# Kernel tuning notes

Measured on AMD Instinct MI355X. Metric: run time of the kernel, lower is better.

## Reference

```python
import jax, jax.numpy as jnp
import numpy as np
import math

D_MODEL = 1024
NUM_HEADS = 16
ALPHA, BETA, K_SCALE, C_THRESHOLD = 0.7, 0.3, 5.0, 0.3
TAU_SCHEDULE = [0.05, 0.05, 0.05, 0.15, 0.25, 0.35, 0.45, 0.55, 0.65, 0.7, 0.75, 0.8]


def setup_inputs() -> dict:
    key = jax.random.key(0)
    ks = jax.random.split(key, 6)
    B, S = 2, 1024
    scale = D_MODEL ** -0.5
    return {
        "x": jax.random.normal(ks[0], (B, S, D_MODEL), dtype=jnp.float32),
        "entropy_prev": jax.random.uniform(ks[1], (B, NUM_HEADS, S, 1), dtype=jnp.float32),
        "Wq": jax.random.normal(ks[2], (D_MODEL, D_MODEL), dtype=jnp.float32) * scale,
        "Wk": jax.random.normal(ks[3], (D_MODEL, D_MODEL), dtype=jnp.float32) * scale,
        "Wv": jax.random.normal(ks[4], (D_MODEL, D_MODEL), dtype=jnp.float32) * scale,
        "Wo": jax.random.normal(ks[5], (D_MODEL, D_MODEL), dtype=jnp.float32) * scale,
        "layer_idx": 4,
    }


def _proj(x, W, B, S, H, Dh):
    # nn.Linear(bias=False): y = x @ W.T ; then [B,S,H,Dh] -> [B,H,S,Dh]
    return jnp.einsum('bsd,ed->bse', x, W).reshape(B, S, H, Dh).transpose(0, 2, 1, 3)


def reference(x, entropy_prev, Wq, Wk, Wv, Wo, layer_idx):
    B, S, _ = x.shape
    H = NUM_HEADS
    Dh = D_MODEL // H
    tau = TAU_SCHEDULE[int(layer_idx)]

    Q = _proj(x, Wq, B, S, H, Dh)
    K = _proj(x, Wk, B, S, H, Dh)
    V = _proj(x, Wv, B, S, H, Dh)

    # raw scores [B,H,S,S]
    scores_raw = jnp.einsum('bhqd,bhkd->bhqk', Q, K) / math.sqrt(Dh)

    # key salience [B,H,1,S]
    sal = jnp.minimum((K * K).sum(axis=-1) / float(Dh), 2.0)
    sal_b = sal[:, :, None, :]

    # WIPER gate [B,H,S,S] (entropy_prev broadcasts over key dim)
    E_t = jax.nn.sigmoid(K_SCALE * (entropy_prev - C_THRESHOLD))
    gate_logit = jnp.clip(E_t * 5.0 + ALPHA * sal_b * 2.0 - BETA * entropy_prev * 1.0, -20.0, 20.0)
    gate = jax.nn.sigmoid(gate_logit)

    mask = gate >= tau
    scores_gated = jnp.where(mask, scores_raw + jnp.log(gate + 1e-8), -jnp.inf)

    best_k_idx = jnp.argmax(scores_raw, axis=-1)  # [B,H,S]
    any_finite = mask.any(axis=-1, keepdims=True)  # [B,H,S,1]

    # safe softmax: degenerate (all -inf) rows replaced by 0s, result discarded below
    attn_raw = jax.nn.softmax(jnp.where(any_finite, scores_gated, 0.0), axis=-1)
    keep_one = jax.nn.one_hot(best_k_idx, S, dtype=x.dtype)
    attn = jnp.where(any_finite, attn_raw, keep_one)

    O = jnp.einsum('bhqk,bhkd->bhqd', attn, V)

    # entropy state: S = log(l) - E[s']
    max_scores = scores_gated.max(axis=-1, keepdims=True)
    shifted = scores_gated - max_scores
    fm = jnp.isfinite(shifted)
    shifted_safe = jnp.where(fm, shifted, 0.0)
    exp_scores = jnp.where(fm, jnp.exp(shifted_safe), 0.0)
    l = jnp.maximum(exp_scores.sum(axis=-1, keepdims=True), 1e-20)
    weighted = (exp_scores * shifted_safe).sum(axis=-1, keepdims=True)
    S_state = jnp.where(any_finite, jnp.log(l) - weighted / l, 0.0)

    out = jnp.einsum('bsd,ed->bse', O.transpose(0, 2, 1, 3).reshape(B, S, D_MODEL), Wo)
    return out, S_state
```

## Files before the change

### kernel.cpp

```cpp
#include <hip/hip_runtime.h>
#include <cstdint>

#define DEVINL __device__ __forceinline__

typedef __attribute__((ext_vector_type(8))) short bf16x8;
typedef __attribute__((ext_vector_type(4))) float f32x4;
typedef __attribute__((ext_vector_type(8))) unsigned short u16x8;
typedef unsigned short u16;
typedef unsigned int u32;

#define MFMA16(a, b, c) __builtin_amdgcn_mfma_f32_16x16x32_bf16(a, b, c, 0, 0, 0)

#define LOG2E 1.4426950408889634f
#define LN2 0.69314718055994531f

DEVINL u16 f2bf(float x) {
  u32 u = __builtin_bit_cast(u32, x);
  u += 0x7FFFu + ((u >> 16) & 1u);
  return (u16)(u >> 16);
}
DEVINL float exp2fast(float x) {
  float r;
  asm("v_exp_f32 %0, %1" : "=v"(r) : "v"(x));
  return r;
}
DEVINL void gload_lds16(const void* g, void* l) {
  __builtin_amdgcn_global_load_lds(
      (const __attribute__((address_space(1))) unsigned int*)g,
      (__attribute__((address_space(3))) unsigned int*)l, 16, 0, 0);
}

__global__ __launch_bounds__(256) void k_prep(const float* __restrict__ x,
                                              const float* __restrict__ Wq,
                                              const float* __restrict__ Wk,
                                              const float* __restrict__ Wv,
                                              const float* __restrict__ Wo,
                                              const float* __restrict__ ent,
                                              u16* __restrict__ xb,
                                              u16* __restrict__ Wb,
                                              u16* __restrict__ Wob,
                                              float* __restrict__ efq) {
  const int bid = blockIdx.x;
  if (bid < 3072) {
    const float* src;
    u16* dst;
    int base;
    if (bid < 1024)      { src = x;  dst = xb;            base = bid; }
    else if (bid < 1536) { src = Wq; dst = Wb;            base = bid - 1024; }
    else if (bid < 2048) { src = Wk; dst = Wb + (1u<<20); base = bid - 1536; }
    else if (bid < 2560) { src = Wv; dst = Wb + (2u<<20); base = bid - 2048; }
    else                 { src = Wo; dst = Wob;           base = bid - 2560; }
    int i = base * 256 + threadIdx.x;
    const float4* s4 = (const float4*)src;
    float4 a = s4[2 * i], b = s4[2 * i + 1];
    u16x8 o;
    o[0] = f2bf(a.x); o[1] = f2bf(a.y); o[2] = f2bf(a.z); o[3] = f2bf(a.w);
    o[4] = f2bf(b.x); o[5] = f2bf(b.y); o[6] = f2bf(b.z); o[7] = f2bf(b.w);
    *(u16x8*)(dst + 8 * i) = o;
  } else {
    int i = (bid - 3072) * 256 + threadIdx.x;
    float e = ent[i];
    float Et = 1.f / (1.f + __expf(-5.f * (e - 0.3f)));
    efq[i] = __expf(-(5.f * Et - 0.3f * e));
  }
}

template <int BM, int BN, int NDIM, int MODE>
__global__ __launch_bounds__(256) void k_gemm(const u16* __restrict__ A,
                                              const u16* __restrict__ Bw,
                                              int Kdim, u16* __restrict__ Qo,
                                              u16* __restrict__ Ko,
                                              u16* __restrict__ Vt,
                                              float* __restrict__ egk_out,
                                              float* __restrict__ Cout) {
  constexpr int MT = BM / 32, NT = BN / 32;
  constexpr int MB = 2048 / BM, NB = NDIM / BN;
  constexpr int CPX = MB * NB / 8;
  __shared__ __align__(16) u16 SM[2][(BM + BN) * 64];
  const int t = threadIdx.x;
  const int lb = (blockIdx.x & 7) * CPX + (blockIdx.x >> 3);
  const int m0 = (lb % MB) * BM, n0 = (lb / MB) * BN;
  const int lane = t & 63, w = t >> 6;
  const int wr = w >> 1, wc = w & 1, lm = lane & 15, lg = lane >> 4;
  const int rs = t >> 3, cs = t & 7;
  f32x4 acc[MT][NT] = {};

#define GSTAGE(buf, kt)                                                        \
  {                                                                            \
    u16* As_ = SM[buf];                                                        \
    u16* Bs_ = SM[buf] + BM * 64;                                              \
    _Pragma("unroll") for (int i = 0; i < BM / 32; ++i) {                      \
      int rr = rs + 32 * i;                                                    \
      gload_lds16(A + (size_t)(m0 + rr) * Kdim + (kt) + ((cs ^ (rr & 7)) * 8), \
                  (char*)As_ + t * 16 + i * 4096);                             \
    }                                                                          \
    _Pragma("unroll") for (int i = 0; i < BN / 32; ++i) {                      \
      int rr = rs + 32 * i;                                                    \
      gload_lds16(Bw + (size_t)(n0 + rr) * Kdim + (kt) + ((cs ^ (rr & 7)) * 8),\
                  (char*)Bs_ + t * 16 + i * 4096);                             \
    }                                                                          \
  }

  GSTAGE(0, 0);
  __syncthreads();
  const int nk = Kdim >> 6;
  for (int ki = 0; ki < nk; ++ki) {
    const int cur = ki & 1;
    if (ki + 1 < nk) GSTAGE(cur ^ 1, (ki + 1) * 64);
    const u16* As = SM[cur];
    const u16* Bs = SM[cur] + BM * 64;
#pragma unroll
    for (int ks = 0; ks < 2; ++ks) {
      bf16x8 af[MT], bfr[NT];
#pragma unroll
      for (int mt = 0; mt < MT; ++mt) {
        int row = wr * (BM / 2) + mt * 16 + lm;
        af[mt] = *(const bf16x8*)((const char*)As + row * 128 +
                                  (((ks * 4 + lg) ^ (row & 7)) << 4));
      }
#pragma unroll
      for (int nt = 0; nt < NT; ++nt) {
        int row = wc * (BN / 2) + nt * 16 + lm;
        bfr[nt] = *(const bf16x8*)((const char*)Bs + row * 128 +
                                   (((ks * 4 + lg) ^ (row & 7)) << 4));
      }
#pragma unroll
      for (int mt = 0; mt < MT; ++mt)
#pragma unroll
        for (int nt = 0; nt < NT; ++nt)
          acc[mt][nt] = MFMA16(af[mt], bfr[nt], acc[mt][nt]);
    }
    __syncthreads();
  }
#undef GSTAGE

  if (MODE == 1) {
#pragma unroll
    for (int mt = 0; mt < MT; ++mt)
#pragma unroll
      for (int nt = 0; nt < NT; ++nt)
#pragma unroll
        for (int r = 0; r < 4; ++r) {
          int m = m0 + wr * (BM / 2) + mt * 16 + lg * 4 + r;
          int n = n0 + wc * (BN / 2) + nt * 16 + lm;
          Cout[(size_t)m * 1024 + n] = acc[mt][nt][r];
        }
    return;
  }

  const int region = n0 >> 10;
  const int b = m0 >> 10, s0 = m0 & 1023;
  if (region < 2) {
    u16* dst = region == 0 ? Qo : Ko;
    const float scl = region == 0 ? 0.125f * LOG2E : 1.f;
#pragma unroll
    for (int mt = 0; mt < MT; ++mt)
#pragma unroll
      for (int nt = 0; nt < NT; ++nt)
#pragma unroll
        for (int r = 0; r < 4; ++r) {
          int m = m0 + wr * (BM / 2) + mt * 16 + lg * 4 + r;
          int n = n0 + wc * (BN / 2) + nt * 16 + lm;
          int e = n & 1023, h = e >> 6, d = e & 63;
          dst[(size_t)(((b << 4) + h) * 1024 + (m & 1023)) * 64 + d] =
              f2bf(acc[mt][nt][r] * scl);
        }
    if (region == 1) {
      int hh = ((n0 - 1024) >> 6) + wc;
#pragma unroll
      for (int mt = 0; mt < MT; ++mt)
#pragma unroll
        for (int r = 0; r < 4; ++r) {
          float ss = 0.f;
#pragma unroll
          for (int nt = 0; nt < NT; ++nt) ss += acc[mt][nt][r] * acc[mt][nt][r];
          ss += __shfl_xor(ss, 1);
          ss += __shfl_xor(ss, 2);
          ss += __shfl_xor(ss, 4);
          ss += __shfl_xor(ss, 8);
          if (lm == 0) {
            int s = s0 + wr * (BM / 2) + mt * 16 + lg * 4 + r;
            float g = 1.4f * fminf(ss * (1.f / 64.f), 2.f);
            egk_out[(size_t)(((b << 4) + hh)) * 1024 + s] = __expf(-g);
          }
        }
    }
  } else {
    u16* tile = SM[0];
#pragma unroll
    for (int half = 0; half < 2; ++half) {
      if (wc == half) {
#pragma unroll
        for (int mt = 0; mt < MT; ++mt)
#pragma unroll
          for (int nt = 0; nt < NT; ++nt)
#pragma unroll
            for (int r = 0; r < 4; ++r) {
              int d = nt * 16 + lm;
              int mloc = wr * (BM / 2) + mt * 16 + lg * 4 + r;
              tile[d * 64 + (mloc ^ ((d & 7) << 3))] = f2bf(acc[mt][nt][r]);
            }
      }
      __syncthreads();
      int hh = ((n0 - 2048) >> 6) + half;
#pragma unroll
      for (int j = 0; j < 2; ++j) {
        int dd = (t >> 3) + 32 * j, mc = t & 7;
        u16x8 v = *(const u16x8*)&tile[dd * 64 + ((mc * 8) ^ ((dd & 7) << 3))];
        *(u16x8*)(Vt + ((size_t)(((b << 4) + hh) * 64 + dd)) * 1024 + s0 + mc * 8) = v;
      }
      __syncthreads();
    }
  }
}

__global__ __launch_bounds__(256, 2) void k_attn(const u16* __restrict__ Q,
                                                 const u16* __restrict__ Kt,
                                                 const u16* __restrict__ Vt,
                                                 const float* __restrict__ efq,
                                                 const float* __restrict__ egk,
                                                 u16* __restrict__ Ob,
                                                 float* __restrict__ Sst) {
  __shared__ __align__(16) u16 Ks[2][128 * 64];
  __shared__ __align__(16) u16 Vs[2][64 * 128];
  __shared__ __align__(16) u32 Ps[4][16][64];
  const int i = blockIdx.x;
  const int lb = ((i & 7) << 6) | (i >> 3);
  const int bh = lb >> 4, qblk = lb & 15;
  const int t = threadIdx.x, lane = t & 63, w = t >> 6;
  const int lm = lane & 15, lg = lane >> 4;
  const int b = bh >> 4, h = bh & 15;
  const size_t bhS = (size_t)bh << 10;
  const int qb = qblk * 64 + w * 16;

#define STAGE(buf, k0)                                                         \
  {                                                                            \
    int rowK = t >> 3, cK = t & 7;                                             \
    int rowV = t >> 4, cV = t & 15;                                            \
    _Pragma("unroll") for (int i2 = 0; i2 < 4; ++i2) {                         \
      int rr = rowK + 32 * i2;                                                 \
      gload_lds16(Kt + (bhS + (k0) + rr) * 64 + ((cK ^ (rr & 7)) * 8),         \
                  (char*)Ks[buf] + t * 16 + i2 * 4096);                        \
      int dd2 = rowV + 16 * i2;                                                \
      gload_lds16(Vt + ((size_t)bh * 64 + dd2) * 1024 + (k0) +                 \
                      ((cV ^ (dd2 & 15)) * 8),                                 \
                  (char*)Vs[buf] + t * 16 + i2 * 4096);                        \
    }                                                                          \
  }

  bf16x8 qf[2];
#pragma unroll
  for (int ks = 0; ks < 2; ++ks)
    qf[ks] = *(const bf16x8*)(Q + (bhS + qb + lm) * 64 + ks * 32 + lg * 8);
  const float efql = efq[bhS + qb + lm];

  f32x4 Oacc[4] = {};
  float m_r = -1e30f, l_r = 0.f, W_r = 0.f;

  STAGE(0, 0);
  f32x4 egN[8];
#pragma unroll
  for (int nt = 0; nt < 8; ++nt)
    egN[nt] = *(const f32x4*)&egk[bhS + nt * 16 + lg * 4];
  __syncthreads();

  for (int kt = 0; kt < 8; ++kt) {
    const int cur = kt & 1;
    if (kt < 7) STAGE(cur ^ 1, (kt + 1) * 128);

    f32x4 c_[8];
    __builtin_amdgcn_s_setprio(1);
#pragma unroll
    for (int nt = 0; nt < 8; ++nt) {
      c_[nt] = (f32x4){0.f, 0.f, 0.f, 0.f};
#pragma unroll
      for (int ks = 0; ks < 2; ++ks) {
        int row = nt * 16 + lm;
        int byo = (((ks * 4 + lg) ^ (row & 7)) << 4);
        bf16x8 kb = *(const bf16x8*)((const char*)Ks[cur] + row * 128 + byo);
        c_[nt] = MFMA16(kb, qf[ks], c_[nt]);
      }
    }
    __builtin_amdgcn_s_setprio(0);

    float v_[8][4];
    float lmax = -3e38f;
#pragma unroll
    for (int nt = 0; nt < 8; ++nt) {
      f32x4 eg = egN[nt];
#pragma unroll
      for (int r = 0; r < 4; ++r) {
        float xg = efql * eg[r];
        float t3 = fmaf(xg, 0.37f, -0.72134752f);
        float lp = xg * fmaf(xg, t3, 1.4426950f);
        v_[nt][r] = c_[nt][r] - lp;
      }
      lmax = fmaxf(fmaxf(lmax, v_[nt][0]),
                   fmaxf(fmaxf(v_[nt][1], v_[nt][2]), v_[nt][3]));
    }
    if (kt < 7) {
#pragma unroll
      for (int nt = 0; nt < 8; ++nt)
        egN[nt] = *(const f32x4*)&egk[bhS + (kt + 1) * 128 + nt * 16 + lg * 4];
    }
    lmax = fmaxf(lmax, __shfl_xor(lmax, 16));
    lmax = fmaxf(lmax, __shfl_xor(lmax, 32));

    if (__any(lmax > m_r + 7.2134752f)) {
      float mn = fmaxf(m_r, lmax);
      float dd = m_r - mn;
      float sc = exp2fast(dd);
      W_r = sc * (W_r + dd * l_r);
      l_r *= sc;
      m_r = mn;
      float scO[4];
#pragma unroll
      for (int r = 0; r < 4; ++r) scO[r] = __shfl(sc, (lane & 48) | (lg * 4 + r));
#pragma unroll
      for (int dt = 0; dt < 4; ++dt)
#pragma unroll
        for (int r = 0; r < 4; ++r) Oacc[dt][r] *= scO[r];
    }

    float psumR[4] = {0.f, 0.f, 0.f, 0.f}, wsumR[4] = {0.f, 0.f, 0.f, 0.f};
    u32 pw[16];
#pragma unroll
    for (int nt = 0; nt < 8; ++nt) {
      float p_[4];
#pragma unroll
      for (int r = 0; r < 4; ++r) {
        float sh = v_[nt][r] - m_r;
        float p = exp2fast(sh);
        p_[r] = p;
        psumR[r] += p;
        wsumR[r] = fmaf(p, sh, wsumR[r]);
      }
      asm("v_cvt_pk_bf16_f32 %0, %1, %2" : "=v"(pw[nt * 2 + 0]) : "v"(p_[0]), "v"(p_[1]));
      asm("v_cvt_pk_bf16_f32 %0, %1, %2" : "=v"(pw[nt * 2 + 1]) : "v"(p_[2]), "v"(p_[3]));
    }
    float psum = (psumR[0] + psumR[1]) + (psumR[2] + psumR[3]);
    float wsum = (wsumR[0] + wsumR[1]) + (wsumR[2] + wsumR[3]);
    psum += __shfl_xor(psum, 16);
    psum += __shfl_xor(psum, 32);
    wsum += __shfl_xor(wsum, 16);
    wsum += __shfl_xor(wsum, 32);
    l_r += psum;
    W_r += wsum;

    u32* prow = &Ps[w][lm][0];
    const int sw = (lm & 7) << 2;
#pragma unroll
    for (int nt = 0; nt < 8; ++nt) {
      int idx = (nt * 8 + lg * 2) ^ sw;
      uint2 pr;
      pr.x = pw[nt * 2 + 0];
      pr.y = pw[nt * 2 + 1];
      *(uint2*)(prow + idx) = pr;
    }

    bf16x8 pa[4];
#pragma unroll
    for (int ks = 0; ks < 4; ++ks) {
      int idx = (ks * 16 + lg * 4) ^ sw;
      pa[ks] = *(const bf16x8*)(prow + idx);
    }
    __builtin_amdgcn_s_setprio(1);
#pragma unroll
    for (int dt = 0; dt < 4; ++dt) {
#pragma unroll
      for (int ks = 0; ks < 4; ++ks) {
        int row = dt * 16 + lm;
        int byo = (((ks * 4 + lg) ^ (row & 15)) << 4);
        bf16x8 vb = *(const bf16x8*)((const char*)Vs[cur] + row * 256 + byo);
        Oacc[dt] = MFMA16(pa[ks], vb, Oacc[dt]);
      }
    }
    __builtin_amdgcn_s_setprio(0);
    __syncthreads();
  }

  float invl = 1.f / l_r;
  float entv = __logf(l_r) - (W_r * LN2) * invl;
  float invO[4];
#pragma unroll
  for (int r = 0; r < 4; ++r) invO[r] = __shfl(invl, (lane & 48) | (lg * 4 + r));
#pragma unroll
  for (int dt = 0; dt < 4; ++dt)
#pragma unroll
    for (int r = 0; r < 4; ++r) {
      int srow = qb + lg * 4 + r;
      int col = h * 64 + dt * 16 + lm;
      Ob[(size_t)(b * 1024 + srow) * 1024 + col] = f2bf(Oacc[dt][r] * invO[r]);
    }
  if (lg == 0) Sst[bhS + qb + lm] = entv;
#undef STAGE
}

static constexpr size_t OFF_XB = 0;
static constexpr size_t OFF_WB = 4ull << 20;
static constexpr size_t OFF_Q = 10ull << 20;
static constexpr size_t OFF_K = 14ull << 20;
static constexpr size_t OFF_OB = 18ull << 20;
static constexpr size_t OFF_VT = 22ull << 20;
static constexpr size_t OFF_WOB = 26ull << 20;
static constexpr size_t OFF_FQ = 28ull << 20;
static constexpr size_t OFF_GK = (28ull << 20) + (128ull << 10);

extern "C" void kernel_launch(void* const* d_in, const int* in_sizes, int n_in,
                              void* d_out, int out_size, void* d_ws, size_t ws_size,
                              hipStream_t stream) {
  const float* x = (const float*)d_in[0];
  const float* ent = (const float*)d_in[1];
  const float* Wq = (const float*)d_in[2];
  const float* Wk = (const float*)d_in[3];
  const float* Wv = (const float*)d_in[4];
  const float* Wo = (const float*)d_in[5];
  (void)in_sizes; (void)n_in; (void)out_size; (void)ws_size;

  char* ws = (char*)d_ws;
  u16* xb = (u16*)(ws + OFF_XB);
  u16* Wb = (u16*)(ws + OFF_WB);
  u16* Qb = (u16*)(ws + OFF_Q);
  u16* Kb = (u16*)(ws + OFF_K);
  u16* Ob = (u16*)(ws + OFF_OB);
  u16* Vtb = (u16*)(ws + OFF_VT);
  u16* Wob = (u16*)(ws + OFF_WOB);
  float* efqd = (float*)(ws + OFF_FQ);
  float* egkd = (float*)(ws + OFF_GK);
  float* outp = (float*)d_out;
  float* Sst = outp + 2u * 1024u * 1024u;

  k_prep<<<3200, 256, 0, stream>>>(x, Wq, Wk, Wv, Wo, ent, xb, Wb, Wob, efqd);

  k_gemm<64, 128, 3072, 0><<<768, 256, 0, stream>>>(xb, Wb, 1024, Qb, Kb, Vtb,
                                                    egkd, nullptr);

  k_attn<<<512, 256, 0, stream>>>(Qb, Kb, Vtb, efqd, egkd, Ob, Sst);

  k_gemm<64, 64, 1024, 1><<<512, 256, 0, stream>>>(Ob, Wob, 1024, nullptr, nullptr,
                                                   nullptr, nullptr, outp);
}
```

Measured before the change: 66.78 us.

## Split attention key range across wave pairs and merge partial softmax states

The attention kernel now handles 32 queries per block. Each pair of waves splits every 128-key tile into two 64-key halves, and the partial max, sum, weighted-sum and O accumulators are merged through shared memory at the end. The grid doubles to 1024 blocks. Double buffering of K/V is dropped in favor of a single staged buffer with a sync per tile, which cuts LDS use and allows 4 blocks per CU. This aims to raise occupancy and parallelism, at the cost of exposed load latency, an extra merge step, and K/V being reloaded by twice as many blocks.

Measured after the change: 68.21 us. 1.02x slower.

```diff
diff --git a/kernel.cpp b/kernel.cpp
--- a/kernel.cpp
+++ b/kernel.cpp
@@ -214,39 +214,44 @@
   }
 }
 
-__global__ __launch_bounds__(256, 2) void k_attn(const u16* __restrict__ Q,
-                                                 const u16* __restrict__ Kt,
-                                                 const u16* __restrict__ Vt,
-                                                 const float* __restrict__ efq,
-                                                 const float* __restrict__ egk,
-                                                 u16* __restrict__ Ob,
-                                                 float* __restrict__ Sst) {
-  __shared__ __align__(16) u16 Ks[2][128 * 64];
-  __shared__ __align__(16) u16 Vs[2][64 * 128];
-  __shared__ __align__(16) u32 Ps[4][16][64];
+__global__ __launch_bounds__(256, 4) void k_attn2(const u16* __restrict__ Q,
+                                                  const u16* __restrict__ Kt,
+                                                  const u16* __restrict__ Vt,
+                                                  const float* __restrict__ efq,
+                                                  const float* __restrict__ egk,
+                                                  u16* __restrict__ Ob,
+                                                  float* __restrict__ Sst) {
+  __shared__ __align__(16) u16 Ks[128 * 64];
+  __shared__ __align__(16) u16 Vs[2][64 * 64];
+  __shared__ __align__(16) u32 Ps[4][16][32];
   const int i = blockIdx.x;
-  const int lb = ((i & 7) << 6) | (i >> 3);
-  const int bh = lb >> 4, qblk = lb & 15;
+  const int lb = ((i & 7) << 7) | (i >> 3);
+  const int bh = lb >> 5, qpb = lb & 31;
   const int t = threadIdx.x, lane = t & 63, w = t >> 6;
   const int lm = lane & 15, lg = lane >> 4;
   const int b = bh >> 4, h = bh & 15;
   const size_t bhS = (size_t)bh << 10;
-  const int qb = qblk * 64 + w * 16;
-
-#define STAGE(buf, k0)                                                         \
-  {                                                                            \
-    int rowK = t >> 3, cK = t & 7;                                             \
-    int rowV = t >> 4, cV = t & 15;                                            \
-    _Pragma("unroll") for (int i2 = 0; i2 < 4; ++i2) {                         \
-      int rr = rowK + 32 * i2;                                                 \
-      gload_lds16(Kt + (bhS + (k0) + rr) * 64 + ((cK ^ (rr & 7)) * 8),         \
-                  (char*)Ks[buf] + t * 16 + i2 * 4096);                        \
-      int dd2 = rowV + 16 * i2;                                                \
-      gload_lds16(Vt + ((size_t)bh * 64 + dd2) * 1024 + (k0) +                 \
-                      ((cV ^ (dd2 & 15)) * 8),                                 \
-                  (char*)Vs[buf] + t * 16 + i2 * 4096);                        \
-    }                                                                          \
-  }
+  const int khalf = w & 1, qt = w >> 1;
+  const int qb = qpb * 32 + qt * 16;
+
+  auto stage = [&](int k0) {
+    int rowK = t >> 3, cK = t & 7;
+#pragma unroll
+    for (int i2 = 0; i2 < 4; ++i2) {
+      int rr = rowK + 32 * i2;
+      gload_lds16(Kt + (bhS + k0 + rr) * 64 + ((cK ^ (rr & 7)) * 8),
+                  (char*)Ks + t * 16 + i2 * 4096);
+    }
+#pragma unroll
+    for (int half = 0; half < 2; ++half)
+#pragma unroll
+      for (int i2 = 0; i2 < 2; ++i2) {
+        int dd = rowK + 32 * i2;
+        gload_lds16(Vt + ((size_t)bh * 64 + dd) * 1024 + k0 + half * 64 +
+                        ((cK ^ (dd & 7)) * 8),
+                    (char*)Vs[half] + t * 16 + i2 * 4096);
+      }
+  };
 
   bf16x8 qf[2];
 #pragma unroll
@@ -257,36 +262,36 @@
   f32x4 Oacc[4] = {};
   float m_r = -1e30f, l_r = 0.f, W_r = 0.f;
 
-  STAGE(0, 0);
-  f32x4 egN[8];
-#pragma unroll
-  for (int nt = 0; nt < 8; ++nt)
-    egN[nt] = *(const f32x4*)&egk[bhS + nt * 16 + lg * 4];
-  __syncthreads();
-
-  for (int kt = 0; kt < 8; ++kt) {
-    const int cur = kt & 1;
-    if (kt < 7) STAGE(cur ^ 1, (kt + 1) * 128);
-
-    f32x4 c_[8];
+  for (int jt = 0; jt < 8; ++jt) {
+    stage(jt * 128);
+    __syncthreads();
+
+    const int kbase = khalf * 64;
+    f32x4 egN[4];
+#pragma unroll
+    for (int nt = 0; nt < 4; ++nt)
+      egN[nt] = *(const f32x4*)&egk[bhS + jt * 128 + kbase + nt * 16 + lg * 4];
+
+    f32x4 c_[4];
     __builtin_amdgcn_s_setprio(1);
 #pragma unroll
-    for (int nt = 0; nt < 8; ++nt) {
+    for (int nt = 0; nt < 4; ++nt) {
       c_[nt] = (f32x4){0.f, 0.f, 0.f, 0.f};
 #pragma unroll
       for (int ks = 0; ks < 2; ++ks) {
         int row = nt * 16 + lm;
         int byo = (((ks * 4 + lg) ^ (row & 7)) << 4);
-        bf16x8 kb = *(const bf16x8*)((const char*)Ks[cur] + row * 128 + byo);
+        bf16x8 kb =
+            *(const bf16x8*)((const char*)Ks + (kbase + row) * 128 + byo);
         c_[nt] = MFMA16(kb, qf[ks], c_[nt]);
       }
     }
     __builtin_amdgcn_s_setprio(0);
 
-    float v_[8][4];
+    float v_[4][4];
     float lmax = -3e38f;
 #pragma unroll
-    for (int nt = 0; nt < 8; ++nt) {
+    for (int nt = 0; nt < 4; ++nt) {
       f32x4 eg = egN[nt];
 #pragma unroll
       for (int r = 0; r < 4; ++r) {
@@ -297,11 +302,6 @@
       }
       lmax = fmaxf(fmaxf(lmax, v_[nt][0]),
                    fmaxf(fmaxf(v_[nt][1], v_[nt][2]), v_[nt][3]));
-    }
-    if (kt < 7) {
-#pragma unroll
-      for (int nt = 0; nt < 8; ++nt)
-        egN[nt] = *(const f32x4*)&egk[bhS + (kt + 1) * 128 + nt * 16 + lg * 4];
     }
     lmax = fmaxf(lmax, __shfl_xor(lmax, 16));
     lmax = fmaxf(lmax, __shfl_xor(lmax, 32));
@@ -323,9 +323,9 @@
     }
 
     float psumR[4] = {0.f, 0.f, 0.f, 0.f}, wsumR[4] = {0.f, 0.f, 0.f, 0.f};
-    u32 pw[16];
-#pragma unroll
-    for (int nt = 0; nt < 8; ++nt) {
+    u32 pw[8];
+#pragma unroll
+    for (int nt = 0; nt < 4; ++nt) {
       float p_[4];
 #pragma unroll
       for (int r = 0; r < 4; ++r) {
@@ -335,8 +335,8 @@
         psumR[r] += p;
         wsumR[r] = fmaf(p, sh, wsumR[r]);
       }
-      asm("v_cvt_pk_bf16_f32 %0, %1, %2" : "=v"(pw[nt * 2 + 0]) : "v"(p_[0]), "v"(p_[1]));
-      asm("v_cvt_pk_bf16_f32 %0, %1, %2" : "=v"(pw[nt * 2 + 1]) : "v"(p_[2]), "v"(p_[3]));
+      asm("v_cvt_pk_bf16_f32 %0, %1, %2" : "=v"(pw[nt*2+0]) : "v"(p_[0]), "v"(p_[1]));
+      asm("v_cvt_pk_bf16_f32 %0, %1, %2" : "=v"(pw[nt*2+1]) : "v"(p_[2]), "v"(p_[3]));
     }
     float psum = (psumR[0] + psumR[1]) + (psumR[2] + psumR[3]);
     float wsum = (wsumR[0] + wsumR[1]) + (wsumR[2] + wsumR[3]);
@@ -350,7 +350,7 @@
     u32* prow = &Ps[w][lm][0];
     const int sw = (lm & 7) << 2;
 #pragma unroll
-    for (int nt = 0; nt < 8; ++nt) {
+    for (int nt = 0; nt < 4; ++nt) {
       int idx = (nt * 8 + lg * 2) ^ sw;
       uint2 pr;
       pr.x = pw[nt * 2 + 0];
@@ -358,9 +358,9 @@
       *(uint2*)(prow + idx) = pr;
     }
 
-    bf16x8 pa[4];
-#pragma unroll
-    for (int ks = 0; ks < 4; ++ks) {
+    bf16x8 pa[2];
+#pragma unroll
+    for (int ks = 0; ks < 2; ++ks) {
       int idx = (ks * 16 + lg * 4) ^ sw;
       pa[ks] = *(const bf16x8*)(prow + idx);
     }
@@ -368,10 +368,11 @@
 #pragma unroll
     for (int dt = 0; dt < 4; ++dt) {
 #pragma unroll
-      for (int ks = 0; ks < 4; ++ks) {
+      for (int ks = 0; ks < 2; ++ks) {
         int row = dt * 16 + lm;
-        int byo = (((ks * 4 + lg) ^ (row & 15)) << 4);
-        bf16x8 vb = *(const bf16x8*)((const char*)Vs[cur] + row * 256 + byo);
+        int byo = (((ks * 4 + lg) ^ (row & 7)) << 4);
+        bf16x8 vb =
+            *(const bf16x8*)((const char*)Vs[khalf] + row * 128 + byo);
         Oacc[dt] = MFMA16(pa[ks], vb, Oacc[dt]);
       }
     }
@@ -379,21 +380,47 @@
     __syncthreads();
   }
 
-  float invl = 1.f / l_r;
-  float entv = __logf(l_r) - (W_r * LN2) * invl;
-  float invO[4];
-#pragma unroll
-  for (int r = 0; r < 4; ++r) invO[r] = __shfl(invl, (lane & 48) | (lg * 4 + r));
-#pragma unroll
-  for (int dt = 0; dt < 4; ++dt)
+  float* mrg = (float*)Ks + qt * 1088;
+  if (khalf == 1) {
+#pragma unroll
+    for (int dt = 0; dt < 4; ++dt)
+#pragma unroll
+      for (int r = 0; r < 4; ++r) mrg[(dt * 4 + r) * 64 + lane] = Oacc[dt][r];
+    if (lg == 0) {
+      mrg[1024 + lm] = m_r;
+      mrg[1040 + lm] = l_r;
+      mrg[1056 + lm] = W_r;
+    }
+  }
+  __syncthreads();
+  if (khalf == 0) {
+    float m1 = mrg[1024 + lm], l1 = mrg[1040 + lm], W1 = mrg[1056 + lm];
+    float mn = fmaxf(m_r, m1);
+    float s0 = exp2fast(m_r - mn), s1 = exp2fast(m1 - mn);
+    float l = l_r * s0 + l1 * s1;
+    float W = s0 * (W_r + (m_r - mn) * l_r) + s1 * (W1 + (m1 - mn) * l1);
+    float invl = 1.f / l;
+    float entv = __logf(l) - (W * LN2) * invl;
+    float s0q[4], s1q[4], invq[4];
 #pragma unroll
     for (int r = 0; r < 4; ++r) {
-      int srow = qb + lg * 4 + r;
-      int col = h * 64 + dt * 16 + lm;
-      Ob[(size_t)(b * 1024 + srow) * 1024 + col] = f2bf(Oacc[dt][r] * invO[r]);
-    }
-  if (lg == 0) Sst[bhS + qb + lm] = entv;
-#undef STAGE
+      int src = (lane & 48) | (lg * 4 + r);
+      s0q[r] = __shfl(s0, src);
+      s1q[r] = __shfl(s1, src);
+      invq[r] = __shfl(invl, src);
+    }
+#pragma unroll
+    for (int dt = 0; dt < 4; ++dt)
+#pragma unroll
+      for (int r = 0; r < 4; ++r) {
+        float o1 = mrg[(dt * 4 + r) * 64 + lane];
+        float o = (Oacc[dt][r] * s0q[r] + o1 * s1q[r]) * invq[r];
+        int srow = qb + lg * 4 + r;
+        int col = h * 64 + dt * 16 + lm;
+        Ob[(size_t)(b * 1024 + srow) * 1024 + col] = f2bf(o);
+      }
+    if (lg == 0) Sst[bhS + qb + lm] = entv;
+  }
 }
 
 static constexpr size_t OFF_XB = 0;
@@ -435,7 +462,7 @@
   k_gemm<64, 128, 3072, 0><<<768, 256, 0, stream>>>(xb, Wb, 1024, Qb, Kb, Vtb,
                                                     egkd, nullptr);
 
-  k_attn<<<512, 256, 0, stream>>>(Qb, Kb, Vtb, efqd, egkd, Ob, Sst);
+  k_attn2<<<1024, 256, 0, stream>>>(Qb, Kb, Vtb, efqd, egkd, Ob, Sst);
 
   k_gemm<64, 64, 1024, 1><<<512, 256, 0, stream>>>(Ob, Wob, 1024, nullptr, nullptr,
                                                    nullptr, nullptr, outp);
```
